# Kernel optimization log

Hardware: AMD Instinct MI355X
Metric: run time of the kernel (lower is better)

## Reference

```python
import jax, jax.numpy as jnp
import numpy as np

B, M, IN, H = 4096, 16, 512, 512


def _linear_params(key, out_dim, in_dim):
    kw, kb = jax.random.split(key)
    s = 1.0 / np.sqrt(in_dim)
    W = jax.random.uniform(kw, (out_dim, in_dim), jnp.float32, -s, s)
    b = jax.random.uniform(kb, (out_dim,), jnp.float32, -s, s)
    return W, b


def setup_inputs() -> dict:
    key = jax.random.key(0)
    ks = jax.random.split(key, 15)
    inp = {
        "input": jax.random.normal(ks[0], (B, IN), jnp.float32),
        "h0": jax.random.normal(ks[1], (B, H), jnp.float32),
        "c0": jax.random.normal(ks[2], (B, H), jnp.float32),
        "all_c_b_e_w": jax.random.normal(ks[3], (B, M, H), jnp.float32),
        "all_num_word": jax.random.randint(ks[4], (B,), 0, M + 1, jnp.int32),
    }
    names = ["ii", "hi", "if_", "hf", "ig", "hg", "io", "ho", "lx", "lc"]
    in_dims = [IN, H, IN, H, IN, H, IN, H, IN, H]
    for n, d, k in zip(names, in_dims, ks[5:15]):
        W, b = _linear_params(k, H, d)
        inp["W_" + n] = W
        inp["b_" + n] = b
    return inp


def _lin(x, W, b):
    return x @ W.T + b


def reference(input, h0, c0, all_c_b_e_w, all_num_word,
              W_ii, b_ii, W_hi, b_hi, W_if_, b_if_, W_hf, b_hf,
              W_ig, b_ig, W_hg, b_hg, W_io, b_io, W_ho, b_ho,
              W_lx, b_lx, W_lc, b_lc):
    i = jax.nn.sigmoid(_lin(input, W_ii, b_ii) + _lin(h0, W_hi, b_hi))   # [B,H]
    f = jax.nn.sigmoid(_lin(input, W_if_, b_if_) + _lin(h0, W_hf, b_hf))  # computed but unused, as in original
    g = jnp.tanh(_lin(input, W_ig, b_ig) + _lin(h0, W_hg, b_hg))         # [B,H]
    o = jax.nn.sigmoid(_lin(input, W_io, b_io) + _lin(h0, W_ho, b_ho))   # [B,H]

    # lattice word-cell gates, vectorized over the ragged word dim with a mask
    lx = _lin(input, W_lx, b_lx)                 # [B,H]
    lc = _lin(all_c_b_e_w, W_lc, b_lc)           # [B,M,H]
    i_b = jax.nn.sigmoid(lx[:, None, :] + lc)    # [B,M,H]
    mask = (jnp.arange(M)[None, :] < all_num_word[:, None])  # [B,M]
    exp_b = jnp.exp(i_b) * mask[:, :, None].astype(i_b.dtype)  # [B,M,H]
    exp_i = jnp.exp(i)                                         # [B,H]
    denom = exp_i + jnp.sum(exp_b, axis=1)                     # [B,H]
    c_words = jnp.sum((exp_b / denom[:, None, :]) * all_c_b_e_w, axis=1)
    c_lat = c_words + (exp_i / denom) * g
    c = jnp.where((all_num_word > 0)[:, None], c_lat, g)       # num_word==0 -> c=g
    h1 = o * jnp.tanh(c)
    return (h1, c)
```

## Files before the change

### kernel.cpp

```cpp
#include <hip/hip_runtime.h>
#include <hip/hip_bf16.h>
#include <stdint.h>


typedef __attribute__((ext_vector_type(8))) short short8;
typedef __attribute__((ext_vector_type(4))) float f32x4;
typedef __attribute__((ext_vector_type(4))) unsigned short us4;

__device__ __forceinline__ unsigned short f2bf(float f) {
  union { float f; unsigned u; } v; v.f = f;
  return (unsigned short)((v.u + 0x7fffu + ((v.u >> 16) & 1u)) >> 16);
}
__device__ __forceinline__ unsigned short f2bf_h(float f) {
  __hip_bfloat16 h = __float2bfloat16(f);
  return *reinterpret_cast<unsigned short*>(&h);
}
__device__ __forceinline__ float bf2f(unsigned short u) {
  return __uint_as_float((unsigned)u << 16);
}
__device__ __forceinline__ float sigmoidf_(float x) {
  return 1.f / (1.f + __expf(-x));
}
__device__ __forceinline__ float fast_tanh(float x) {
  float e = __expf(-2.f * fmaxf(x, -30.f));
  return (1.f - e) / (1.f + e);
}

__global__ void k_cvt_all(const float* __restrict__ x, const float* __restrict__ h,
                          const float* __restrict__ Wii, const float* __restrict__ Wig,
                          const float* __restrict__ Wio, const float* __restrict__ Wlx,
                          const float* __restrict__ Whi, const float* __restrict__ Whg,
                          const float* __restrict__ Who, const float* __restrict__ Wlcf,
                          unsigned short* __restrict__ XH, unsigned short* __restrict__ Wcat,
                          unsigned short* __restrict__ Wlc) {
  const int bb = blockIdx.x;
  const int tid = threadIdx.x;
  us4 o;
  if (bb < 4096) {
    const int t = bb * 256 + tid;
    const int b = t >> 8;
    const int col = (t & 255) * 4;
    const float* src = (col < 512) ? (x + (size_t)b * 512 + col)
                                   : (h + (size_t)b * 512 + (col - 512));
    f32x4 v = *(const f32x4*)src;
    o[0] = f2bf(v[0]); o[1] = f2bf(v[1]); o[2] = f2bf(v[2]); o[3] = f2bf(v[3]);
    *(us4*)(XH + (size_t)t * 4) = o;
  } else if (bb < 6144) {
    const int t = (bb - 4096) * 256 + tid;
    const int row = t >> 8;
    const int col = (t & 255) * 4;
    const int sec = row >> 9, r = row & 511;
    if (col < 512) {
      const float* W = sec == 0 ? Wii : sec == 1 ? Wig : sec == 2 ? Wio : Wlx;
      f32x4 v = *(const f32x4*)(W + (size_t)r * 512 + col);
      o[0] = f2bf(v[0]); o[1] = f2bf(v[1]); o[2] = f2bf(v[2]); o[3] = f2bf(v[3]);
    } else if (sec < 3) {
      const float* W = sec == 0 ? Whi : sec == 1 ? Whg : Who;
      f32x4 v = *(const f32x4*)(W + (size_t)r * 512 + (col - 512));
      o[0] = f2bf(v[0]); o[1] = f2bf(v[1]); o[2] = f2bf(v[2]); o[3] = f2bf(v[3]);
    } else {
      o[0] = 0; o[1] = 0; o[2] = 0; o[3] = 0;
    }
    *(us4*)(Wcat + (size_t)t * 4) = o;
  } else {
    const int t = (bb - 6144) * 256 + tid;
    f32x4 v = *(const f32x4*)(Wlcf + (size_t)t * 4);
    o[0] = f2bf(v[0]); o[1] = f2bf(v[1]); o[2] = f2bf(v[2]); o[3] = f2bf(v[3]);
    *(us4*)(Wlc + (size_t)t * 4) = o;
  }
}

__global__ __launch_bounds__(256) void k_gemm0(
    const unsigned short* __restrict__ A, const unsigned short* __restrict__ Bm,
    unsigned short* __restrict__ C, int Ndim, int Kdim, int nbx) {
  __shared__ unsigned short As[2][128 * 64];
  __shared__ unsigned short Bs[2][128 * 64];
  const int tid = threadIdx.x;
  const int lane = tid & 63, wid = tid >> 6;
  const int wr = wid >> 1, wc = wid & 1;
  const int l15 = lane & 15, lhi = lane >> 4;

  const int chunk = gridDim.x >> 3;
  const int bid = (blockIdx.x & 7) * chunk + (blockIdx.x >> 3);
  const int brow = bid / nbx, bcol = bid % nbx;
  const int m0 = brow * 128, n0 = bcol * 128;

  f32x4 acc[4][4];
#pragma unroll
  for (int i = 0; i < 4; ++i)
#pragma unroll
    for (int j = 0; j < 4; ++j) acc[i][j] = (f32x4){0.f, 0.f, 0.f, 0.f};

  const int cb0 = wid * 64;
  auto stage = [&](int buf, int k0) {
#pragma unroll
    for (int q = 0; q < 4; ++q) {
      const int cb = q * 256 + cb0;
      const int chunkid = cb + lane;
      const int row = chunkid >> 3, slot = chunkid & 7;
      const int kk = k0 + ((slot ^ (row & 7)) << 3);
      __builtin_amdgcn_global_load_lds(
          (const __attribute__((address_space(1))) unsigned int*)(A + (size_t)(m0 + row) * Kdim + kk),
          (__attribute__((address_space(3))) unsigned int*)(As[buf] + cb * 8), 16, 0, 0);
      __builtin_amdgcn_global_load_lds(
          (const __attribute__((address_space(1))) unsigned int*)(Bm + (size_t)(n0 + row) * Kdim + kk),
          (__attribute__((address_space(3))) unsigned int*)(Bs[buf] + cb * 8), 16, 0, 0);
    }
  };

  const int nt = Kdim >> 6;
  stage(0, 0);
  __syncthreads();

  const int swz = (lane & 7) << 4;
  for (int t = 0; t < nt; ++t) {
    const int cur = t & 1;
    if (t + 1 < nt) stage(cur ^ 1, (t + 1) << 6);
    const char* Ab = (const char*)As[cur];
    const char* Bb = (const char*)Bs[cur];
#pragma unroll
    for (int s = 0; s < 2; ++s) {
      short8 av[4], bv[4];
#pragma unroll
      for (int mi = 0; mi < 4; ++mi) {
        const int row = wr * 64 + mi * 16 + l15;
        av[mi] = *(const short8*)(Ab + row * 128 + ((s * 64 + lhi * 16) ^ swz));
      }
#pragma unroll
      for (int ni = 0; ni < 4; ++ni) {
        const int row = wc * 64 + ni * 16 + l15;
        bv[ni] = *(const short8*)(Bb + row * 128 + ((s * 64 + lhi * 16) ^ swz));
      }
#pragma unroll
      for (int mi = 0; mi < 4; ++mi)
#pragma unroll
        for (int ni = 0; ni < 4; ++ni)
          acc[mi][ni] = __builtin_amdgcn_mfma_f32_16x16x32_bf16(av[mi], bv[ni], acc[mi][ni], 0, 0, 0);
    }
    __syncthreads();
  }

#pragma unroll
  for (int mi = 0; mi < 4; ++mi) {
    const int gr = m0 + wr * 64 + mi * 16 + lhi * 4;
#pragma unroll
    for (int ni = 0; ni < 4; ++ni) {
      const int gc = n0 + wc * 64 + ni * 16 + l15;
#pragma unroll
      for (int j = 0; j < 4; ++j)
        C[(size_t)(gr + j) * Ndim + gc] = f2bf(acc[mi][ni][j]);
    }
  }
}

__global__ __launch_bounds__(512) void k_latg(
    const float* __restrict__ Af,
    const unsigned short* __restrict__ Bm,
    const unsigned short* __restrict__ C1u,
    const int* __restrict__ num_word,
    const float* __restrict__ b_ii, const float* __restrict__ b_hi,
    const float* __restrict__ b_ig, const float* __restrict__ b_hg,
    const float* __restrict__ b_io, const float* __restrict__ b_ho,
    const float* __restrict__ b_lx, const float* __restrict__ b_lc,
    float* __restrict__ outH, float* __restrict__ outC) {
  __shared__ unsigned short As[2][256 * 32];
  __shared__ unsigned short Bs[2][256 * 32];
  const int tid = threadIdx.x;
  const int lane = tid & 63, wid = tid >> 6;
  const int wrow = wid >> 2, wcol = wid & 3;
  const int l15 = lane & 15, lhi = lane >> 4;

  const int chunk = gridDim.x >> 3;
  const int bid = (blockIdx.x & 7) * chunk + (blockIdx.x >> 3);
  const int brow = bid >> 1, bcol = bid & 1;
  const int m0 = brow * 256, n0 = bcol * 256;

  f32x4 acc[8][4];
#pragma unroll
  for (int i = 0; i < 8; ++i)
#pragma unroll
    for (int j = 0; j < 4; ++j) acc[i][j] = (f32x4){0.f, 0.f, 0.f, 0.f};

  f32x4 SA[2][2], SB[2][2];

  auto loadA = [&](f32x4 (&dst)[2][2], int k0) {
#pragma unroll
    for (int q = 0; q < 2; ++q) {
      const int c = q * 512 + tid;
      const int row = c >> 2, s = c & 3;
      const float* p = Af + (size_t)(m0 + row) * 512 + k0 + s * 8;
      dst[q][0] = *(const f32x4*)p;
      dst[q][1] = *(const f32x4*)(p + 4);
    }
  };
  auto writeA = [&](int buf, f32x4 (&src)[2][2]) {
#pragma unroll
    for (int q = 0; q < 2; ++q) {
      const int c = q * 512 + tid;
      const int row = c >> 2, s = c & 3;
      const int pr = row >> 1;
      const int phys = (s + ((row & 1) << 2)) ^ (pr & 7);
      short8 v;
      v[0] = (short)f2bf_h(src[q][0][0]); v[1] = (short)f2bf_h(src[q][0][1]);
      v[2] = (short)f2bf_h(src[q][0][2]); v[3] = (short)f2bf_h(src[q][0][3]);
      v[4] = (short)f2bf_h(src[q][1][0]); v[5] = (short)f2bf_h(src[q][1][1]);
      v[6] = (short)f2bf_h(src[q][1][2]); v[7] = (short)f2bf_h(src[q][1][3]);
      *(short8*)((char*)As[buf] + pr * 128 + phys * 16) = v;
    }
  };
  auto stageB = [&](int buf, int k0) {
#pragma unroll
    for (int q = 0; q < 2; ++q) {
      const int cb = q * 512 + wid * 64;
      const int c = cb + lane;
      const int pr = c >> 3, phys = c & 7;
      const int gi = phys ^ (pr & 7);
      const int row = pr * 2 + (gi >> 2);
      const int kk = k0 + ((gi & 3) << 3);
      __builtin_amdgcn_global_load_lds(
          (const __attribute__((address_space(1))) unsigned int*)(Bm + (size_t)(n0 + row) * 512 + kk),
          (__attribute__((address_space(3))) unsigned int*)(Bs[buf] + cb * 8), 16, 0, 0);
    }
  };

  auto compute = [&](int buf) {
    const char* Ab = (const char*)As[buf];
    const char* Bb = (const char*)Bs[buf];
    short8 av[8], bv[4];
#pragma unroll
    for (int mi = 0; mi < 8; ++mi) {
      const int row = wrow * 128 + mi * 16 + l15;
      const int pr = row >> 1;
      av[mi] = *(const short8*)(Ab + pr * 128 +
                (((lhi + ((row & 1) << 2)) ^ (pr & 7)) << 4));
    }
#pragma unroll
    for (int ni = 0; ni < 4; ++ni) {
      const int row = wcol * 64 + ni * 16 + l15;
      const int pr = row >> 1;
      bv[ni] = *(const short8*)(Bb + pr * 128 +
                (((lhi + ((row & 1) << 2)) ^ (pr & 7)) << 4));
    }
#pragma unroll
    for (int mi = 0; mi < 8; ++mi)
#pragma unroll
      for (int ni = 0; ni < 4; ++ni)
        acc[mi][ni] = __builtin_amdgcn_mfma_f32_16x16x32_bf16(av[mi], bv[ni], acc[mi][ni], 0, 0, 0);
  };

  loadA(SA, 0);
  loadA(SB, 32);
  stageB(0, 0);
  writeA(0, SA);
  __syncthreads();

#pragma unroll 1
  for (int t = 0; t < 16; t += 2) {
    if (t + 2 < 16) loadA(SA, (t + 2) << 5);
    if (t + 1 < 16) stageB(1, (t + 1) << 5);
    compute(0);
    if (t + 1 < 16) writeA(1, SB);
    __syncthreads();
    if (t + 3 < 16) loadA(SB, (t + 3) << 5);
    if (t + 2 < 16) stageB(0, (t + 2) << 5);
    compute(1);
    if (t + 2 < 16) writeA(0, SA);
    __syncthreads();
  }

  const int b0 = m0 >> 4;
#pragma unroll
  for (int ni = 0; ni < 4; ++ni) {
    const int hc = n0 + wcol * 64 + ni * 16 + l15;
    const float pre0 = b_lx[hc] + b_lc[hc];
    const float bI = b_ii[hc] + b_hi[hc];
    const float bG = b_ig[hc] + b_hg[hc];
    const float bO = b_io[hc] + b_ho[hc];
#pragma unroll
    for (int mi = 0; mi < 8; ++mi) {
      const int b = b0 + wrow * 8 + mi;
      const int nw = num_word[b];
      const size_t base = (size_t)b * 2048;
      const float pre = bf2f(C1u[base + 1536 + hc]) + pre0;
      float se = 0.f, sew = 0.f;
#pragma unroll
      for (int j = 0; j < 4; ++j) {
        const int m = lhi * 4 + j;
        const float ib = sigmoidf_(pre + acc[mi][ni][j]);
        const float e = (m < nw) ? __expf(ib) : 0.f;
        const float w = Af[((size_t)b * 16 + m) * 512 + hc];
        se += e;
        sew += e * w;
      }
      se += __shfl_xor(se, 16, 64);
      sew += __shfl_xor(sew, 16, 64);
      se += __shfl_xor(se, 32, 64);
      sew += __shfl_xor(sew, 32, 64);
      if (lhi == 0) {
        const float ig = sigmoidf_(bf2f(C1u[base + hc]) + bI);
        const float g  = fast_tanh(bf2f(C1u[base + 512 + hc]) + bG);
        const float og = sigmoidf_(bf2f(C1u[base + 1024 + hc]) + bO);
        const float ei = __expf(ig);
        const float denom = ei + se;
        const float cc = (sew + ei * g) / denom;
        outH[(size_t)b * 512 + hc] = og * fast_tanh(cc);
        outC[(size_t)b * 512 + hc] = cc;
      }
    }
  }
}

extern "C" void kernel_launch(void* const* d_in, const int* in_sizes, int n_in,
                              void* d_out, int out_size, void* d_ws, size_t ws_size,
                              hipStream_t stream) {
  const float* input    = (const float*)d_in[0];
  const float* h0       = (const float*)d_in[1];
  const float* all_c    = (const float*)d_in[3];
  const int*   num_word = (const int*)d_in[4];
  const float* W_ii = (const float*)d_in[5];  const float* b_ii = (const float*)d_in[6];
  const float* W_hi = (const float*)d_in[7];  const float* b_hi = (const float*)d_in[8];
  const float* W_ig = (const float*)d_in[13]; const float* b_ig = (const float*)d_in[14];
  const float* W_hg = (const float*)d_in[15]; const float* b_hg = (const float*)d_in[16];
  const float* W_io = (const float*)d_in[17]; const float* b_io = (const float*)d_in[18];
  const float* W_ho = (const float*)d_in[19]; const float* b_ho = (const float*)d_in[20];
  const float* W_lx = (const float*)d_in[21]; const float* b_lx = (const float*)d_in[22];
  const float* W_lc = (const float*)d_in[23]; const float* b_lc = (const float*)d_in[24];

  char* ws = (char*)d_ws;
  unsigned short* XH   = (unsigned short*)(ws);
  unsigned short* Wcat = (unsigned short*)(ws + 8388608);
  unsigned short* Wlc  = (unsigned short*)(ws + 12582912);
  unsigned short* C1u  = (unsigned short*)(ws + 13107200);

  float* outH = (float*)d_out;
  float* outC = outH + (size_t)4096 * 512;

  k_cvt_all<<<6400, 256, 0, stream>>>(input, h0, W_ii, W_ig, W_io, W_lx,
                                      W_hi, W_hg, W_ho, W_lc, XH, Wcat, Wlc);

  k_gemm0<<<512, 256, 0, stream>>>(XH, Wcat, C1u, 2048, 1024, 16);

  k_latg<<<512, 512, 0, stream>>>(all_c, Wlc, C1u, num_word,
      b_ii, b_hi, b_ig, b_hg, b_io, b_ho, b_lx, b_lc, outH, outC);
}
```

Measured before the change: 138.8 us.

## Run gate GEMM and lattice GEMM concurrently in one kernel, split epilogue

Merges the gate GEMM and the lattice word-cell GEMM into one 1024-block launch that interleaves the two kinds of blocks, so the independent GEMMs can run at the same time instead of one after another. The lattice epilogue is moved into a separate per-batch kernel. That kernel reads a bf16 lc intermediate, which is written only for valid words, and loops only over num_word entries. This removes the dependency that made the lattice GEMM wait for the gate GEMM, but it adds a round trip of the lc tensor through global memory and a third launch. Gate blocks leave half their threads idle and only calling __syncthreads in a loop.

New measurement: 125.8 us, median of 2. 9.3% less time.

```diff
diff --git a/kernel.cpp b/kernel.cpp
--- a/kernel.cpp
+++ b/kernel.cpp
@@ -70,110 +70,104 @@
   }
 }
 
-__global__ __launch_bounds__(256) void k_gemm0(
-    const unsigned short* __restrict__ A, const unsigned short* __restrict__ Bm,
-    unsigned short* __restrict__ C, int Ndim, int Kdim, int nbx) {
-  __shared__ unsigned short As[2][128 * 64];
-  __shared__ unsigned short Bs[2][128 * 64];
+__global__ __launch_bounds__(512) void k_mega(
+    const float* __restrict__ Af,
+    const unsigned short* __restrict__ Wlc,
+    unsigned short* __restrict__ lcb,
+    const int* __restrict__ num_word,
+    const unsigned short* __restrict__ XH,
+    const unsigned short* __restrict__ Wcat,
+    unsigned short* __restrict__ C1u) {
+  __shared__ unsigned short smem[32768];
   const int tid = threadIdx.x;
   const int lane = tid & 63, wid = tid >> 6;
-  const int wr = wid >> 1, wc = wid & 1;
   const int l15 = lane & 15, lhi = lane >> 4;
 
   const int chunk = gridDim.x >> 3;
-  const int bid = (blockIdx.x & 7) * chunk + (blockIdx.x >> 3);
-  const int brow = bid / nbx, bcol = bid % nbx;
-  const int m0 = brow * 128, n0 = bcol * 128;
-
-  f32x4 acc[4][4];
-#pragma unroll
-  for (int i = 0; i < 4; ++i)
-#pragma unroll
-    for (int j = 0; j < 4; ++j) acc[i][j] = (f32x4){0.f, 0.f, 0.f, 0.f};
-
-  const int cb0 = wid * 64;
-  auto stage = [&](int buf, int k0) {
-#pragma unroll
-    for (int q = 0; q < 4; ++q) {
-      const int cb = q * 256 + cb0;
-      const int chunkid = cb + lane;
-      const int row = chunkid >> 3, slot = chunkid & 7;
-      const int kk = k0 + ((slot ^ (row & 7)) << 3);
-      __builtin_amdgcn_global_load_lds(
-          (const __attribute__((address_space(1))) unsigned int*)(A + (size_t)(m0 + row) * Kdim + kk),
-          (__attribute__((address_space(3))) unsigned int*)(As[buf] + cb * 8), 16, 0, 0);
-      __builtin_amdgcn_global_load_lds(
-          (const __attribute__((address_space(1))) unsigned int*)(Bm + (size_t)(n0 + row) * Kdim + kk),
-          (__attribute__((address_space(3))) unsigned int*)(Bs[buf] + cb * 8), 16, 0, 0);
-    }
-  };
-
-  const int nt = Kdim >> 6;
-  stage(0, 0);
-  __syncthreads();
-
-  const int swz = (lane & 7) << 4;
-  for (int t = 0; t < nt; ++t) {
-    const int cur = t & 1;
-    if (t + 1 < nt) stage(cur ^ 1, (t + 1) << 6);
-    const char* Ab = (const char*)As[cur];
-    const char* Bb = (const char*)Bs[cur];
-#pragma unroll
-    for (int s = 0; s < 2; ++s) {
-      short8 av[4], bv[4];
+  const int bid2 = (blockIdx.x & 7) * chunk + (blockIdx.x >> 3);
+
+  if (bid2 & 1) {
+    const int gid = bid2 >> 1;
+    const int brow = gid >> 4, bcol = gid & 15;
+    const int m0 = brow * 128, n0 = bcol * 128;
+    unsigned short* As = smem;
+    unsigned short* Bs = smem + 16384;
+    if (tid < 256) {
+      const int wr = wid >> 1, wc = wid & 1;
+      f32x4 acc[4][4];
+#pragma unroll
+      for (int i = 0; i < 4; ++i)
+#pragma unroll
+        for (int j = 0; j < 4; ++j) acc[i][j] = (f32x4){0.f, 0.f, 0.f, 0.f};
+
+      auto stage0 = [&](int buf, int k0) {
+#pragma unroll
+        for (int q = 0; q < 4; ++q) {
+          const int cb = q * 256 + wid * 64;
+          const int c = cb + lane;
+          const int row = c >> 3, slot = c & 7;
+          const int kk = k0 + ((slot ^ (row & 7)) << 3);
+          __builtin_amdgcn_global_load_lds(
+              (const __attribute__((address_space(1))) unsigned int*)(XH + (size_t)(m0 + row) * 1024 + kk),
+              (__attribute__((address_space(3))) unsigned int*)(As + buf * 8192 + cb * 8), 16, 0, 0);
+          __builtin_amdgcn_global_load_lds(
+              (const __attribute__((address_space(1))) unsigned int*)(Wcat + (size_t)(n0 + row) * 1024 + kk),
+              (__attribute__((address_space(3))) unsigned int*)(Bs + buf * 8192 + cb * 8), 16, 0, 0);
+        }
+      };
+
+      stage0(0, 0);
+      __syncthreads();
+      const int swz = (lane & 7) << 4;
+      for (int t = 0; t < 16; ++t) {
+        const int cur = t & 1;
+        if (t + 1 < 16) stage0(cur ^ 1, (t + 1) << 6);
+        const char* Ab = (const char*)(As + cur * 8192);
+        const char* Bb = (const char*)(Bs + cur * 8192);
+#pragma unroll
+        for (int s = 0; s < 2; ++s) {
+          short8 av[4], bv[4];
+#pragma unroll
+          for (int mi = 0; mi < 4; ++mi) {
+            const int row = wr * 64 + mi * 16 + l15;
+            av[mi] = *(const short8*)(Ab + row * 128 + ((s * 64 + lhi * 16) ^ swz));
+          }
+#pragma unroll
+          for (int ni = 0; ni < 4; ++ni) {
+            const int row = wc * 64 + ni * 16 + l15;
+            bv[ni] = *(const short8*)(Bb + row * 128 + ((s * 64 + lhi * 16) ^ swz));
+          }
+#pragma unroll
+          for (int mi = 0; mi < 4; ++mi)
+#pragma unroll
+            for (int ni = 0; ni < 4; ++ni)
+              acc[mi][ni] = __builtin_amdgcn_mfma_f32_16x16x32_bf16(av[mi], bv[ni], acc[mi][ni], 0, 0, 0);
+        }
+        __syncthreads();
+      }
 #pragma unroll
       for (int mi = 0; mi < 4; ++mi) {
-        const int row = wr * 64 + mi * 16 + l15;
-        av[mi] = *(const short8*)(Ab + row * 128 + ((s * 64 + lhi * 16) ^ swz));
+        const int gr = m0 + wr * 64 + mi * 16 + lhi * 4;
+#pragma unroll
+        for (int ni = 0; ni < 4; ++ni) {
+          const int gc = n0 + wc * 64 + ni * 16 + l15;
+#pragma unroll
+          for (int j = 0; j < 4; ++j)
+            C1u[(size_t)(gr + j) * 2048 + gc] = f2bf(acc[mi][ni][j]);
+        }
       }
-#pragma unroll
-      for (int ni = 0; ni < 4; ++ni) {
-        const int row = wc * 64 + ni * 16 + l15;
-        bv[ni] = *(const short8*)(Bb + row * 128 + ((s * 64 + lhi * 16) ^ swz));
-      }
-#pragma unroll
-      for (int mi = 0; mi < 4; ++mi)
-#pragma unroll
-        for (int ni = 0; ni < 4; ++ni)
-          acc[mi][ni] = __builtin_amdgcn_mfma_f32_16x16x32_bf16(av[mi], bv[ni], acc[mi][ni], 0, 0, 0);
-    }
-    __syncthreads();
-  }
-
-#pragma unroll
-  for (int mi = 0; mi < 4; ++mi) {
-    const int gr = m0 + wr * 64 + mi * 16 + lhi * 4;
-#pragma unroll
-    for (int ni = 0; ni < 4; ++ni) {
-      const int gc = n0 + wc * 64 + ni * 16 + l15;
-#pragma unroll
-      for (int j = 0; j < 4; ++j)
-        C[(size_t)(gr + j) * Ndim + gc] = f2bf(acc[mi][ni][j]);
-    }
-  }
-}
-
-__global__ __launch_bounds__(512) void k_latg(
-    const float* __restrict__ Af,
-    const unsigned short* __restrict__ Bm,
-    const unsigned short* __restrict__ C1u,
-    const int* __restrict__ num_word,
-    const float* __restrict__ b_ii, const float* __restrict__ b_hi,
-    const float* __restrict__ b_ig, const float* __restrict__ b_hg,
-    const float* __restrict__ b_io, const float* __restrict__ b_ho,
-    const float* __restrict__ b_lx, const float* __restrict__ b_lc,
-    float* __restrict__ outH, float* __restrict__ outC) {
-  __shared__ unsigned short As[2][256 * 32];
-  __shared__ unsigned short Bs[2][256 * 32];
-  const int tid = threadIdx.x;
-  const int lane = tid & 63, wid = tid >> 6;
+    } else {
+      for (int i = 0; i < 17; ++i) __syncthreads();
+    }
+    return;
+  }
+
+  const int lid = bid2 >> 1;
+  const int brow = lid >> 1, bcol = lid & 1;
+  const int m0 = brow * 256, n0 = bcol * 256;
   const int wrow = wid >> 2, wcol = wid & 3;
-  const int l15 = lane & 15, lhi = lane >> 4;
-
-  const int chunk = gridDim.x >> 3;
-  const int bid = (blockIdx.x & 7) * chunk + (blockIdx.x >> 3);
-  const int brow = bid >> 1, bcol = bid & 1;
-  const int m0 = brow * 256, n0 = bcol * 256;
+  unsigned short* Asl = smem;
+  unsigned short* Bsl = smem + 16384;
 
   f32x4 acc[8][4];
 #pragma unroll
@@ -205,7 +199,7 @@
       v[2] = (short)f2bf_h(src[q][0][2]); v[3] = (short)f2bf_h(src[q][0][3]);
       v[4] = (short)f2bf_h(src[q][1][0]); v[5] = (short)f2bf_h(src[q][1][1]);
       v[6] = (short)f2bf_h(src[q][1][2]); v[7] = (short)f2bf_h(src[q][1][3]);
-      *(short8*)((char*)As[buf] + pr * 128 + phys * 16) = v;
+      *(short8*)((char*)(Asl + buf * 8192) + pr * 128 + phys * 16) = v;
     }
   };
   auto stageB = [&](int buf, int k0) {
@@ -218,14 +212,13 @@
       const int row = pr * 2 + (gi >> 2);
       const int kk = k0 + ((gi & 3) << 3);
       __builtin_amdgcn_global_load_lds(
-          (const __attribute__((address_space(1))) unsigned int*)(Bm + (size_t)(n0 + row) * 512 + kk),
-          (__attribute__((address_space(3))) unsigned int*)(Bs[buf] + cb * 8), 16, 0, 0);
+          (const __attribute__((address_space(1))) unsigned int*)(Wlc + (size_t)(n0 + row) * 512 + kk),
+          (__attribute__((address_space(3))) unsigned int*)(Bsl + buf * 8192 + cb * 8), 16, 0, 0);
     }
   };
-
   auto compute = [&](int buf) {
-    const char* Ab = (const char*)As[buf];
-    const char* Bb = (const char*)Bs[buf];
+    const char* Ab = (const char*)(Asl + buf * 8192);
+    const char* Bb = (const char*)(Bsl + buf * 8192);
     short8 av[8], bv[4];
 #pragma unroll
     for (int mi = 0; mi < 8; ++mi) {
@@ -268,46 +261,58 @@
     __syncthreads();
   }
 
-  const int b0 = m0 >> 4;
-#pragma unroll
-  for (int ni = 0; ni < 4; ++ni) {
-    const int hc = n0 + wcol * 64 + ni * 16 + l15;
-    const float pre0 = b_lx[hc] + b_lc[hc];
-    const float bI = b_ii[hc] + b_hi[hc];
-    const float bG = b_ig[hc] + b_hg[hc];
-    const float bO = b_io[hc] + b_ho[hc];
-#pragma unroll
-    for (int mi = 0; mi < 8; ++mi) {
-      const int b = b0 + wrow * 8 + mi;
-      const int nw = num_word[b];
-      const size_t base = (size_t)b * 2048;
-      const float pre = bf2f(C1u[base + 1536 + hc]) + pre0;
-      float se = 0.f, sew = 0.f;
-#pragma unroll
-      for (int j = 0; j < 4; ++j) {
-        const int m = lhi * 4 + j;
-        const float ib = sigmoidf_(pre + acc[mi][ni][j]);
-        const float e = (m < nw) ? __expf(ib) : 0.f;
-        const float w = Af[((size_t)b * 16 + m) * 512 + hc];
-        se += e;
-        sew += e * w;
-      }
-      se += __shfl_xor(se, 16, 64);
-      sew += __shfl_xor(sew, 16, 64);
-      se += __shfl_xor(se, 32, 64);
-      sew += __shfl_xor(sew, 32, 64);
-      if (lhi == 0) {
-        const float ig = sigmoidf_(bf2f(C1u[base + hc]) + bI);
-        const float g  = fast_tanh(bf2f(C1u[base + 512 + hc]) + bG);
-        const float og = sigmoidf_(bf2f(C1u[base + 1024 + hc]) + bO);
-        const float ei = __expf(ig);
-        const float denom = ei + se;
-        const float cc = (sew + ei * g) / denom;
-        outH[(size_t)b * 512 + hc] = og * fast_tanh(cc);
-        outC[(size_t)b * 512 + hc] = cc;
-      }
-    }
-  }
+#pragma unroll
+  for (int mi = 0; mi < 8; ++mi) {
+    const int rbase = m0 + wrow * 128 + mi * 16;
+    const int nw = num_word[rbase >> 4];
+    const int gr = rbase + lhi * 4;
+#pragma unroll
+    for (int ni = 0; ni < 4; ++ni) {
+      const int gc = n0 + wcol * 64 + ni * 16 + l15;
+#pragma unroll
+      for (int j = 0; j < 4; ++j)
+        if (lhi * 4 + j < nw)
+          lcb[(size_t)(gr + j) * 512 + gc] = f2bf(acc[mi][ni][j]);
+    }
+  }
+}
+
+__global__ __launch_bounds__(512) void k_epi(
+    const unsigned short* __restrict__ lc,
+    const float* __restrict__ all_c,
+    const unsigned short* __restrict__ C1u,
+    const int* __restrict__ num_word,
+    const float* __restrict__ b_ii, const float* __restrict__ b_hi,
+    const float* __restrict__ b_ig, const float* __restrict__ b_hg,
+    const float* __restrict__ b_io, const float* __restrict__ b_ho,
+    const float* __restrict__ b_lx, const float* __restrict__ b_lc,
+    float* __restrict__ outH, float* __restrict__ outC) {
+  const int b = blockIdx.x;
+  const int hc = threadIdx.x;
+  const int nw = num_word[b];
+  const size_t base = (size_t)b * 2048;
+
+  const float pre = bf2f(C1u[base + 1536 + hc]) + b_lx[hc] + b_lc[hc];
+  const unsigned short* lcp = lc + ((size_t)b * 16) * 512 + hc;
+  const float* wp = all_c + ((size_t)b * 16) * 512 + hc;
+
+  float se = 0.f, sew = 0.f;
+#pragma unroll 4
+  for (int m = 0; m < nw; ++m) {
+    const float ib = sigmoidf_(pre + bf2f(lcp[(size_t)m * 512]));
+    const float e = __expf(ib);
+    se += e;
+    sew += e * wp[(size_t)m * 512];
+  }
+
+  const float ig = sigmoidf_(bf2f(C1u[base + hc]) + b_ii[hc] + b_hi[hc]);
+  const float g  = fast_tanh(bf2f(C1u[base + 512 + hc]) + b_ig[hc] + b_hg[hc]);
+  const float og = sigmoidf_(bf2f(C1u[base + 1024 + hc]) + b_io[hc] + b_ho[hc]);
+  const float ei = __expf(ig);
+  const float denom = ei + se;
+  const float cc = (sew + ei * g) / denom;
+  outH[(size_t)b * 512 + hc] = og * fast_tanh(cc);
+  outC[(size_t)b * 512 + hc] = cc;
 }
 
 extern "C" void kernel_launch(void* const* d_in, const int* in_sizes, int n_in,
@@ -331,6 +336,7 @@
   unsigned short* Wcat = (unsigned short*)(ws + 8388608);
   unsigned short* Wlc  = (unsigned short*)(ws + 12582912);
   unsigned short* C1u  = (unsigned short*)(ws + 13107200);
+  unsigned short* lc   = (unsigned short*)(ws + 29884416);
 
   float* outH = (float*)d_out;
   float* outC = outH + (size_t)4096 * 512;
@@ -338,8 +344,8 @@
   k_cvt_all<<<6400, 256, 0, stream>>>(input, h0, W_ii, W_ig, W_io, W_lx,
                                       W_hi, W_hg, W_ho, W_lc, XH, Wcat, Wlc);
 
-  k_gemm0<<<512, 256, 0, stream>>>(XH, Wcat, C1u, 2048, 1024, 16);
-
-  k_latg<<<512, 512, 0, stream>>>(all_c, Wlc, C1u, num_word,
+  k_mega<<<1024, 512, 0, stream>>>(all_c, Wlc, lc, num_word, XH, Wcat, C1u);
+
+  k_epi<<<4096, 512, 0, stream>>>(lc, all_c, C1u, num_word,
       b_ii, b_hi, b_ig, b_hg, b_io, b_ho, b_lx, b_lc, outH, outC);
 }
```

## Split lattice gate epilogue into separate kernel with masked bf16 lc writes

Applied to the files above, without the earlier changes.

Moves the softmax-style lattice gate epilogue out of the lc GEMM kernel into a new per-batch elementwise kernel. The GEMM now only stores the valid rows of lc as bf16, and the new kernel loops over just num_word entries. This relieves register pressure and epilogue latency in the GEMM and skips masked rows. The cost is an extra launch and a round trip of lc through global memory. It also raises MFMA wave priority around the inner compute loop.

After: 112.2 us, median of 4. 1.24x faster.

```diff
diff --git a/kernel.cpp b/kernel.cpp
--- a/kernel.cpp
+++ b/kernel.cpp
@@ -156,13 +156,8 @@
 __global__ __launch_bounds__(512) void k_latg(
     const float* __restrict__ Af,
     const unsigned short* __restrict__ Bm,
-    const unsigned short* __restrict__ C1u,
     const int* __restrict__ num_word,
-    const float* __restrict__ b_ii, const float* __restrict__ b_hi,
-    const float* __restrict__ b_ig, const float* __restrict__ b_hg,
-    const float* __restrict__ b_io, const float* __restrict__ b_ho,
-    const float* __restrict__ b_lx, const float* __restrict__ b_lc,
-    float* __restrict__ outH, float* __restrict__ outC) {
+    unsigned short* __restrict__ lcb) {
   __shared__ unsigned short As[2][256 * 32];
   __shared__ unsigned short Bs[2][256 * 32];
   const int tid = threadIdx.x;
@@ -241,11 +236,13 @@
       bv[ni] = *(const short8*)(Bb + pr * 128 +
                 (((lhi + ((row & 1) << 2)) ^ (pr & 7)) << 4));
     }
+    __builtin_amdgcn_s_setprio(1);
 #pragma unroll
     for (int mi = 0; mi < 8; ++mi)
 #pragma unroll
       for (int ni = 0; ni < 4; ++ni)
         acc[mi][ni] = __builtin_amdgcn_mfma_f32_16x16x32_bf16(av[mi], bv[ni], acc[mi][ni], 0, 0, 0);
+    __builtin_amdgcn_s_setprio(0);
   };
 
   loadA(SA, 0);
@@ -268,46 +265,58 @@
     __syncthreads();
   }
 
-  const int b0 = m0 >> 4;
-#pragma unroll
-  for (int ni = 0; ni < 4; ++ni) {
-    const int hc = n0 + wcol * 64 + ni * 16 + l15;
-    const float pre0 = b_lx[hc] + b_lc[hc];
-    const float bI = b_ii[hc] + b_hi[hc];
-    const float bG = b_ig[hc] + b_hg[hc];
-    const float bO = b_io[hc] + b_ho[hc];
-#pragma unroll
-    for (int mi = 0; mi < 8; ++mi) {
-      const int b = b0 + wrow * 8 + mi;
-      const int nw = num_word[b];
-      const size_t base = (size_t)b * 2048;
-      const float pre = bf2f(C1u[base + 1536 + hc]) + pre0;
-      float se = 0.f, sew = 0.f;
-#pragma unroll
-      for (int j = 0; j < 4; ++j) {
-        const int m = lhi * 4 + j;
-        const float ib = sigmoidf_(pre + acc[mi][ni][j]);
-        const float e = (m < nw) ? __expf(ib) : 0.f;
-        const float w = Af[((size_t)b * 16 + m) * 512 + hc];
-        se += e;
-        sew += e * w;
-      }
-      se += __shfl_xor(se, 16, 64);
-      sew += __shfl_xor(sew, 16, 64);
-      se += __shfl_xor(se, 32, 64);
-      sew += __shfl_xor(sew, 32, 64);
-      if (lhi == 0) {
-        const float ig = sigmoidf_(bf2f(C1u[base + hc]) + bI);
-        const float g  = fast_tanh(bf2f(C1u[base + 512 + hc]) + bG);
-        const float og = sigmoidf_(bf2f(C1u[base + 1024 + hc]) + bO);
-        const float ei = __expf(ig);
-        const float denom = ei + se;
-        const float cc = (sew + ei * g) / denom;
-        outH[(size_t)b * 512 + hc] = og * fast_tanh(cc);
-        outC[(size_t)b * 512 + hc] = cc;
-      }
-    }
-  }
+#pragma unroll
+  for (int mi = 0; mi < 8; ++mi) {
+    const int rbase = m0 + wrow * 128 + mi * 16;
+    const int nw = num_word[rbase >> 4];
+    const int gr = rbase + lhi * 4;
+#pragma unroll
+    for (int ni = 0; ni < 4; ++ni) {
+      const int gc = n0 + wcol * 64 + ni * 16 + l15;
+#pragma unroll
+      for (int j = 0; j < 4; ++j)
+        if (lhi * 4 + j < nw)
+          lcb[(size_t)(gr + j) * 512 + gc] = f2bf(acc[mi][ni][j]);
+    }
+  }
+}
+
+__global__ __launch_bounds__(512) void k_epi(
+    const unsigned short* __restrict__ lc,
+    const float* __restrict__ all_c,
+    const unsigned short* __restrict__ C1u,
+    const int* __restrict__ num_word,
+    const float* __restrict__ b_ii, const float* __restrict__ b_hi,
+    const float* __restrict__ b_ig, const float* __restrict__ b_hg,
+    const float* __restrict__ b_io, const float* __restrict__ b_ho,
+    const float* __restrict__ b_lx, const float* __restrict__ b_lc,
+    float* __restrict__ outH, float* __restrict__ outC) {
+  const int b = blockIdx.x;
+  const int hc = threadIdx.x;
+  const int nw = num_word[b];
+  const size_t base = (size_t)b * 2048;
+
+  const float pre = bf2f(C1u[base + 1536 + hc]) + b_lx[hc] + b_lc[hc];
+  const unsigned short* lcp = lc + ((size_t)b * 16) * 512 + hc;
+  const float* wp = all_c + ((size_t)b * 16) * 512 + hc;
+
+  float se = 0.f, sew = 0.f;
+#pragma unroll 4
+  for (int m = 0; m < nw; ++m) {
+    const float ib = sigmoidf_(pre + bf2f(lcp[(size_t)m * 512]));
+    const float e = __expf(ib);
+    se += e;
+    sew += e * wp[(size_t)m * 512];
+  }
+
+  const float ig = sigmoidf_(bf2f(C1u[base + hc]) + b_ii[hc] + b_hi[hc]);
+  const float g  = fast_tanh(bf2f(C1u[base + 512 + hc]) + b_ig[hc] + b_hg[hc]);
+  const float og = sigmoidf_(bf2f(C1u[base + 1024 + hc]) + b_io[hc] + b_ho[hc]);
+  const float ei = __expf(ig);
+  const float denom = ei + se;
+  const float cc = (sew + ei * g) / denom;
+  outH[(size_t)b * 512 + hc] = og * fast_tanh(cc);
+  outC[(size_t)b * 512 + hc] = cc;
 }
 
 extern "C" void kernel_launch(void* const* d_in, const int* in_sizes, int n_in,
@@ -331,6 +340,7 @@
   unsigned short* Wcat = (unsigned short*)(ws + 8388608);
   unsigned short* Wlc  = (unsigned short*)(ws + 12582912);
   unsigned short* C1u  = (unsigned short*)(ws + 13107200);
+  unsigned short* lc   = (unsigned short*)(ws + 29884416);
 
   float* outH = (float*)d_out;
   float* outC = outH + (size_t)4096 * 512;
@@ -340,6 +350,8 @@
 
   k_gemm0<<<512, 256, 0, stream>>>(XH, Wcat, C1u, 2048, 1024, 16);
 
-  k_latg<<<512, 512, 0, stream>>>(all_c, Wlc, C1u, num_word,
+  k_latg<<<512, 512, 0, stream>>>(all_c, Wlc, num_word, lc);
+
+  k_epi<<<4096, 512, 0, stream>>>(lc, all_c, C1u, num_word,
       b_ii, b_hi, b_ig, b_hg, b_io, b_ho, b_lx, b_lc, outH, outC);
 }
```
